# Performance work log

Hardware: AMD Instinct MI355X
Metric: run time of the kernel (lower is better)

Reference implementation:

```python
import jax, jax.numpy as jnp
import numpy as np

N_EMBED = 2048
N_HEAD = 16
N_KV_HEAD = 4
HEAD_DIM = N_EMBED // N_HEAD
REPEAT = N_HEAD // N_KV_HEAD
THETA = 10000.0


def setup_inputs() -> dict:
    key = jax.random.key(0)
    ks = jax.random.split(key, 9)
    B, T = 2, 2048
    s = 0.02
    return {
        'x': jax.random.normal(ks[0], (B, T, N_EMBED), jnp.float32),
        'Wq': jax.random.normal(ks[1], (N_EMBED, N_EMBED), jnp.float32) * s,
        'bq': jax.random.normal(ks[2], (N_EMBED,), jnp.float32) * s,
        'Wk': jax.random.normal(ks[3], (N_EMBED, N_KV_HEAD * HEAD_DIM), jnp.float32) * s,
        'bk': jax.random.normal(ks[4], (N_KV_HEAD * HEAD_DIM,), jnp.float32) * s,
        'Wv': jax.random.normal(ks[5], (N_EMBED, N_KV_HEAD * HEAD_DIM), jnp.float32) * s,
        'bv': jax.random.normal(ks[6], (N_KV_HEAD * HEAD_DIM,), jnp.float32) * s,
        'Wo': jax.random.normal(ks[7], (N_EMBED, N_EMBED), jnp.float32) * s,
        'bo': jax.random.normal(ks[8], (N_EMBED,), jnp.float32) * s,
    }


def _rope_angles(T):
    # Quirk of original: freqs exponent uses full n_embed, then sliced to head_dim//2
    freqs = THETA ** (-(jnp.arange(0, N_EMBED, 2, dtype=jnp.float32) / N_EMBED))
    freqs = freqs[: HEAD_DIM // 2]
    t = jnp.arange(T, dtype=jnp.float32)
    return jnp.outer(t, freqs)  # [T, HEAD_DIM//2]


def _apply_rope(x, cos, sin):
    # x: [B, T, H, D]; pairs are adjacent elements along D
    xr = x[..., 0::2]
    xi = x[..., 1::2]
    # cos/sin: [1, T, 1, D//2]
    or_ = xr * cos - xi * sin
    oi_ = xr * sin + xi * cos
    out = jnp.stack([or_, oi_], axis=-1).reshape(x.shape)
    # original casts rope output to bfloat16
    return out.astype(jnp.bfloat16).astype(jnp.float32)


def reference(x, Wq, bq, Wk, bk, Wv, bv, Wo, bo):
    B, T, _ = x.shape
    q = (x @ Wq + bq).reshape(B, T, N_HEAD, HEAD_DIM)
    k = (x @ Wk + bk).reshape(B, T, N_KV_HEAD, HEAD_DIM)
    v = (x @ Wv + bv).reshape(B, T, N_KV_HEAD, HEAD_DIM)

    ang = _rope_angles(T)
    cos = jnp.cos(ang)[None, :, None, :]
    sin = jnp.sin(ang)[None, :, None, :]
    xq = _apply_rope(q, cos, sin)
    xk = _apply_rope(k, cos, sin)

    xq = xq.transpose(0, 2, 1, 3)                 # [B, H, T, D]
    xk = xk.transpose(0, 2, 1, 3)                 # [B, Hkv, T, D]
    xv = v.transpose(0, 2, 1, 3)                  # [B, Hkv, T, D]
    xk = jnp.repeat(xk, REPEAT, axis=1)           # [B, H, T, D]
    xv = jnp.repeat(xv, REPEAT, axis=1)

    qk = jnp.einsum('bhtd,bhsd->bhts', xq, xk)    # [B, H, T, T]
    causal = jnp.tril(jnp.ones((T, T), dtype=bool))
    qk = jnp.where(causal[None, None], qk, -jnp.inf)
    # Quirk: scale applied AFTER softmax, using n_embed**-0.5
    attn = jax.nn.softmax(qk, axis=-1) * (N_EMBED ** -0.5)
    o = jnp.einsum('bhts,bhsd->bhtd', attn, xv)
    o = o.transpose(0, 2, 1, 3).reshape(B, T, N_EMBED)
    return o @ Wo + bo
```

## Files before the change

kernel.cpp:

```cpp
#include <hip/hip_runtime.h>
#include <stdint.h>
#include <math.h>

typedef unsigned short u16;
typedef __attribute__((ext_vector_type(8))) short short8;
typedef __attribute__((ext_vector_type(8))) _Float16 half8;
typedef __attribute__((ext_vector_type(4))) float float4v;
typedef __attribute__((ext_vector_type(16))) float float16v;
typedef __attribute__((ext_vector_type(4))) u16 ushort4v;

#define T_SEQ 2048
#define NB 2
#define NE 2048
#define NH 16
#define NKV 4
#define HD 128
#define KDIM 2048

union Frag { short8 s; half8 h; };

__device__ inline u16 f32_bf16(float f) {
    union { float f; uint32_t u; } v; v.f = f;
    uint32_t u = v.u;
    return (u16)((u + 0x7fffu + ((u >> 16) & 1u)) >> 16);
}
__device__ inline u16 f32_f16(float f) {
    union { _Float16 h; u16 u; } v; v.h = (_Float16)f;
    return v.u;
}

__device__ inline uint32_t cvtpk_bf16(float lo, float hi) {
    uint32_t r;
    asm("v_cvt_pk_bf16_f32 %0, %1, %2" : "=v"(r) : "v"(lo), "v"(hi));
    return r;
}
__device__ inline void perm32swap(uint32_t& a, uint32_t& b) {
    asm("v_permlane32_swap_b32 %0, %1" : "+v"(a), "+v"(b));
}

typedef __attribute__((address_space(1))) const void g_void;
typedef __attribute__((address_space(3))) void l_void;
#define GLOAD16(g, l) __builtin_amdgcn_global_load_lds((g_void*)(g), (l_void*)(l), 16, 0, 0)

__global__ void conv_f16(const float* __restrict__ in, u16* __restrict__ out) {
    int i = blockIdx.x * blockDim.x + threadIdx.x;
    float4 v = ((const float4*)in)[i];
    ushort4v o;
    o.x = f32_f16(v.x); o.y = f32_f16(v.y); o.z = f32_f16(v.z); o.w = f32_f16(v.w);
    *(ushort4v*)(out + (size_t)i * 4) = o;
}

template<bool TO_F16>
__global__ void transpose_convert(const float* __restrict__ in, u16* __restrict__ out,
                                  int K, int N) {
    __shared__ float tile[32][33];
    int n0 = blockIdx.x * 32, k0 = blockIdx.y * 32;
    int tx = threadIdx.x, ty = threadIdx.y;
    for (int i = 0; i < 32; i += 8)
        tile[ty + i][tx] = in[(size_t)(k0 + ty + i) * N + n0 + tx];
    __syncthreads();
    for (int i = 0; i < 32; i += 8) {
        float v = tile[tx][ty + i];
        out[(size_t)(n0 + ty + i) * K + k0 + tx] = TO_F16 ? f32_f16(v) : f32_bf16(v);
    }
}

__global__ void rope_tab(float* __restrict__ ctab, float* __restrict__ stab) {
    int i = blockIdx.x * blockDim.x + threadIdx.x;
    int t = i >> 6, j = i & 63;
    float freqf = (float)pow(10000.0, -(double)j / 1024.0);
    float angf = (float)t * freqf;
    double a = (double)angf;
    ctab[i] = (float)cos(a);
    stab[i] = (float)sin(a);
}

#define GEMM_STAGE_DECL(Asrc, Bsrc) \
    int rin = lane >> 2, ksl = lane & 3; \
    int u0r = wid * 32; \
    const u16* Ag0 = (Asrc) + (size_t)(m0 + u0r + rin) * KDIM + ksl * 8; \
    const u16* Ag1 = (Asrc) + (size_t)(m0 + u0r + 16 + rin) * KDIM + ksl * 8; \
    const u16* Bg0 = (Bsrc) + (size_t)(n0 + u0r + rin) * KDIM + ksl * 8; \
    const u16* Bg1 = (Bsrc) + (size_t)(n0 + u0r + 16 + rin) * KDIM + ksl * 8; \
    u16* Al0 = &Alds[u0r * 32]; \
    u16* Al1 = &Alds[(u0r + 16) * 32]; \
    u16* Bl0 = &Blds[u0r * 32]; \
    u16* Bl1 = &Blds[(u0r + 16) * 32];

#define GEMM_MAINLOOP(F16) \
    for (int k0 = 0; k0 < KDIM; k0 += 32) { \
        __syncthreads(); \
        GLOAD16(Ag0 + k0, Al0); \
        GLOAD16(Ag1 + k0, Al1); \
        GLOAD16(Bg0 + k0, Bl0); \
        GLOAD16(Bg1 + k0, Bl1); \
        __syncthreads(); \
        Frag af[4], bf[4]; \
        for (int i = 0; i < 4; i++) \
            af[i].s = *(const short8*)&Alds[(wr * 64 + i * 16 + l16) * 32 + quad * 8]; \
        for (int j = 0; j < 4; j++) \
            bf[j].s = *(const short8*)&Blds[(wc * 64 + j * 16 + l16) * 32 + quad * 8]; \
        for (int i = 0; i < 4; i++) \
            for (int j = 0; j < 4; j++) { \
                if (F16) \
                    acc[i][j] = __builtin_amdgcn_mfma_f32_16x16x32_f16(af[i].h, bf[j].h, acc[i][j], 0, 0, 0); \
                else \
                    acc[i][j] = __builtin_amdgcn_mfma_f32_16x16x32_bf16(af[i].s, bf[j].s, acc[i][j], 0, 0, 0); \
            } \
    }

__global__ __launch_bounds__(256)
void gemm_qkv(const u16* __restrict__ xh, const u16* __restrict__ wqt,
              const u16* __restrict__ wkt, const u16* __restrict__ wvt,
              const float* __restrict__ bq, const float* __restrict__ bk,
              const float* __restrict__ bv,
              u16* __restrict__ qout, u16* __restrict__ kout, u16* __restrict__ vout,
              const float* __restrict__ ctab, const float* __restrict__ stab) {
    __shared__ u16 Alds[128 * 32];
    __shared__ u16 Blds[128 * 32];
    int tid = threadIdx.x;
    int wid = tid >> 6, lane = tid & 63;
    int quad = lane >> 4, l16 = lane & 15;
    int wr = wid >> 1, wc = wid & 1;

    int lin = blockIdx.x;
    int mode, m0, n0;
    const u16 *A, *Bt;
    if (lin < 512) {
        mode = 0; m0 = (lin >> 4) * 128; n0 = (lin & 15) * 128; A = xh; Bt = wqt;
    } else if (lin < 640) {
        int i = lin - 512;
        mode = 1; m0 = (i >> 2) * 128; n0 = (i & 3) * 128; A = xh; Bt = wkt;
    } else {
        int i = lin - 640;
        mode = 2; m0 = (i & 3) * 128; n0 = (i >> 2) * 128; A = wvt; Bt = xh;
    }

    float4v acc[4][4];
    for (int i = 0; i < 4; i++) for (int j = 0; j < 4; j++) acc[i][j] = (float4v){0,0,0,0};

    GEMM_STAGE_DECL(A, Bt)
    GEMM_MAINLOOP(true)

    if (mode == 2) {
        for (int i = 0; i < 4; i++) {
            int mbase = m0 + wr * 64 + i * 16 + quad * 4;
            float brow[4];
            for (int r = 0; r < 4; r++) brow[r] = bv[mbase + r];
            for (int j = 0; j < 4; j++) {
                int col = n0 + wc * 64 + j * 16 + l16;
                int b = col >> 11, t = col & 2047;
                for (int r = 0; r < 4; r++) {
                    int m = mbase + r;
                    float val = acc[i][j][r] + brow[r];
                    vout[(((size_t)(b * NKV + (m >> 7))) * HD + (m & 127)) * T_SEQ + t] = f32_bf16(val);
                }
            }
        }
    } else {
        const float* bias = mode ? bk : bq;
        u16* outU = mode ? kout : qout;
        int nheads = mode ? NKV : NH;
        for (int i = 0; i < 4; i++) {
            int mbase = m0 + wr * 64 + i * 16 + quad * 4;
            for (int j = 0; j < 4; j++) {
                int col = n0 + wc * 64 + j * 16 + l16;
                float bcol = bias[col];
                for (int r = 0; r < 4; r++) {
                    int m = mbase + r;
                    float val = acc[i][j][r] + bcol;
                    int b = m >> 11, t = m & 2047;
                    int h = col >> 7, d = col & 127;
                    int jj = d >> 1;
                    float c = ctab[t * 64 + jj];
                    float s = stab[t * 64 + jj];
                    float partner = __shfl_xor(val, 1, 64);
                    float o = (d & 1) ? (partner * s + val * c) : (val * c - partner * s);
                    outU[(((size_t)(b * nheads + h)) * T_SEQ + t) * HD + d] = f32_bf16(o);
                }
            }
        }
    }
}

__global__ __launch_bounds__(256)
void gemm_out(const u16* __restrict__ A, const u16* __restrict__ Bt,
              const float* __restrict__ bias, float* __restrict__ outF) {
    __shared__ u16 Alds[128 * 32];
    __shared__ u16 Blds[128 * 32];
    int tid = threadIdx.x;
    int wid = tid >> 6, lane = tid & 63;
    int quad = lane >> 4, l16 = lane & 15;
    int wr = wid >> 1, wc = wid & 1;
    int m0 = blockIdx.x * 128, n0 = blockIdx.y * 128;

    float4v acc[4][4];
    for (int i = 0; i < 4; i++) for (int j = 0; j < 4; j++) acc[i][j] = (float4v){0,0,0,0};

    GEMM_STAGE_DECL(A, Bt)
    GEMM_MAINLOOP(false)

    for (int i = 0; i < 4; i++) {
        int mbase = m0 + wr * 64 + i * 16 + quad * 4;
        for (int j = 0; j < 4; j++) {
            int col = n0 + wc * 64 + j * 16 + l16;
            float bcol = bias[col];
            for (int r = 0; r < 4; r++)
                outF[(size_t)(mbase + r) * NE + col] = acc[i][j][r] + bcol;
        }
    }
}

__global__ __launch_bounds__(256, 2)
void attn_kernel(const u16* __restrict__ Qr, const u16* __restrict__ Kr,
                 const u16* __restrict__ Vt, u16* __restrict__ Oout) {
    __shared__ u16 smem[17920];
    u16* klds = smem;
    u16* vlds = smem + 8704;
    int tid = threadIdx.x;
    int wid = tid >> 6, lane = tid & 63;
    int l32 = lane & 31, hh = lane >> 5;

    int lin = blockIdx.x + (blockIdx.y << 4);
    int g = lin >> 5, bh = lin & 31;
    int qt = (lin < 256) ? (15 - g) : (g - 8);
    int b = bh >> 4, hd = bh & 15, kvh = hd >> 2;
    int t0 = qt * 128;

    const u16* Qb = Qr + (((size_t)(b * NH + hd)) * T_SEQ + t0 + wid * 32) * HD;
    const u16* Kb = Kr + ((size_t)(b * NKV + kvh)) * T_SEQ * HD;
    const u16* Vb = Vt + ((size_t)(b * NKV + kvh)) * HD * T_SEQ;

    short8 qf[8];
#pragma unroll
    for (int ks = 0; ks < 8; ks++)
        qf[ks] = *(const short8*)(Qb + (size_t)l32 * HD + ks * 16 + hh * 8);

    float16v oacc[4];
#pragma unroll
    for (int dt = 0; dt < 4; dt++)
        oacc[dt] = (float16v){0,0,0,0,0,0,0,0,0,0,0,0,0,0,0,0};
    float m_run = -INFINITY, l_run = 0.f;

    int ksr = tid >> 2, kc = (tid & 3) * 32;
    int vdr = tid >> 1, vc = (tid & 1) * 32;

    int nst = 2 * qt + 2;

    {
        const u16* ksrc = Kb + (size_t)ksr * HD + kc;
        const u16* vsrc = Vb + (size_t)vdr * T_SEQ + vc;
        short8 kr0[4], vr0[4];
#pragma unroll
        for (int i = 0; i < 4; i++) kr0[i] = *(const short8*)(ksrc + i * 8);
#pragma unroll
        for (int i = 0; i < 4; i++) vr0[i] = *(const short8*)(vsrc + i * 8);
#pragma unroll
        for (int i = 0; i < 4; i++) *(short8*)&klds[ksr * 136 + kc + i * 8] = kr0[i];
#pragma unroll
        for (int i = 0; i < 4; i++) *(short8*)&vlds[vdr * 72 + vc + i * 8] = vr0[i];
    }
    __syncthreads();

    for (int st = 0; st < nst; st++) {
        short8 krg[4], vrg[4];
        bool more = (st + 1 < nst);
        if (more) {
            const u16* ksrc = Kb + ((size_t)(st + 1) * 64 + ksr) * HD + kc;
            const u16* vsrc = Vb + (size_t)vdr * T_SEQ + (st + 1) * 64 + vc;
#pragma unroll
            for (int i = 0; i < 4; i++) krg[i] = *(const short8*)(ksrc + i * 8);
#pragma unroll
            for (int i = 0; i < 4; i++) vrg[i] = *(const short8*)(vsrc + i * 8);
        }

        bool active = (st * 64) <= (t0 + wid * 32 + 31);
        if (active) {
            float16v sfa[2];
            sfa[0] = (float16v){0,0,0,0,0,0,0,0,0,0,0,0,0,0,0,0};
            sfa[1] = (float16v){0,0,0,0,0,0,0,0,0,0,0,0,0,0,0,0};
            __builtin_amdgcn_s_setprio(1);
#pragma unroll
            for (int ks = 0; ks < 8; ks++) {
                short8 kf0 = *(const short8*)&klds[l32 * 136 + ks * 16 + hh * 8];
                short8 kf1 = *(const short8*)&klds[(32 + l32) * 136 + ks * 16 + hh * 8];
                sfa[0] = __builtin_amdgcn_mfma_f32_32x32x16_bf16(kf0, qf[ks], sfa[0], 0, 0, 0);
                sfa[1] = __builtin_amdgcn_mfma_f32_32x32x16_bf16(kf1, qf[ks], sfa[1], 0, 0, 0);
            }
            __builtin_amdgcn_s_setprio(0);

            int tg = t0 + wid * 32 + l32;
            if (st >= 2 * qt) {
#pragma unroll
                for (int stile = 0; stile < 2; stile++)
#pragma unroll
                    for (int r = 0; r < 16; r++) {
                        int s = st * 64 + stile * 32 + (r & 3) + 8 * (r >> 2) + 4 * hh;
                        if (s > tg) sfa[stile][r] = -INFINITY;
                    }
            }

            float mx = -INFINITY;
#pragma unroll
            for (int stile = 0; stile < 2; stile++)
#pragma unroll
                for (int r = 0; r < 16; r++) mx = fmaxf(mx, sfa[stile][r]);
            mx = fmaxf(mx, __shfl_xor(mx, 32, 64));
            bool nos = __all(mx - m_run <= 8.f);
            float mnew = nos ? m_run : fmaxf(m_run, mx);
            float alpha = nos ? 1.f : __expf(m_run - mnew);
            float psum = 0.f;
#pragma unroll
            for (int stile = 0; stile < 2; stile++)
#pragma unroll
                for (int r = 0; r < 16; r++) {
                    float p = __expf(sfa[stile][r] - mnew);
                    sfa[stile][r] = p;
                    psum += p;
                }
            psum += __shfl_xor(psum, 32, 64);
            l_run = l_run * alpha + psum;
            m_run = mnew;

            if (!nos) {
#pragma unroll
                for (int dt = 0; dt < 4; dt++)
#pragma unroll
                    for (int r = 0; r < 16; r++) oacc[dt][r] *= alpha;
            }

            __builtin_amdgcn_s_setprio(1);
#pragma unroll
            for (int g2 = 0; g2 < 4; g2++) {
                int stile = g2 >> 1, gg = g2 & 1;
                uint32_t P0 = cvtpk_bf16(sfa[stile][8 * gg + 0], sfa[stile][8 * gg + 1]);
                uint32_t P1 = cvtpk_bf16(sfa[stile][8 * gg + 2], sfa[stile][8 * gg + 3]);
                uint32_t P2 = cvtpk_bf16(sfa[stile][8 * gg + 4], sfa[stile][8 * gg + 5]);
                uint32_t P3 = cvtpk_bf16(sfa[stile][8 * gg + 6], sfa[stile][8 * gg + 7]);
                perm32swap(P0, P2);
                perm32swap(P1, P3);
                union { uint32_t w[4]; short8 s; } pf;
                pf.w[0] = P0; pf.w[1] = P1; pf.w[2] = P2; pf.w[3] = P3;
#pragma unroll
                for (int dt = 0; dt < 4; dt++) {
                    short8 vf = *(const short8*)&vlds[(dt * 32 + l32) * 72 + g2 * 16 + hh * 8];
                    oacc[dt] = __builtin_amdgcn_mfma_f32_32x32x16_bf16(vf, pf.s, oacc[dt], 0, 0, 0);
                }
            }
            __builtin_amdgcn_s_setprio(0);
        }

        __syncthreads();
        if (more) {
#pragma unroll
            for (int i = 0; i < 4; i++) *(short8*)&klds[ksr * 136 + kc + i * 8] = krg[i];
#pragma unroll
            for (int i = 0; i < 4; i++) *(short8*)&vlds[vdr * 72 + vc + i * 8] = vrg[i];
        }
        __syncthreads();
    }

    const float scale = 0.022097086912079608f;
    float sc = scale / l_run;
    u16* ow = smem + wid * 4352;
#pragma unroll
    for (int dt = 0; dt < 4; dt++)
#pragma unroll
        for (int gq = 0; gq < 4; gq++) {
            ushort4v pk;
            pk.x = f32_bf16(oacc[dt][gq * 4 + 0] * sc);
            pk.y = f32_bf16(oacc[dt][gq * 4 + 1] * sc);
            pk.z = f32_bf16(oacc[dt][gq * 4 + 2] * sc);
            pk.w = f32_bf16(oacc[dt][gq * 4 + 3] * sc);
            *(ushort4v*)&ow[l32 * 136 + dt * 32 + gq * 8 + hh * 4] = pk;
        }
    __syncthreads();
    int tl = lane >> 4, dcol = (lane & 15) * 8;
#pragma unroll
    for (int ch = 0; ch < 8; ch++) {
        int t_local = tl + ch * 4;
        short8 ov = *(const short8*)&ow[t_local * 136 + dcol];
        *(short8*)&Oout[((size_t)(b * T_SEQ) + t0 + wid * 32 + t_local) * NE + hd * HD + dcol] = ov;
    }
}

extern "C" void kernel_launch(void* const* d_in, const int* in_sizes, int n_in,
                              void* d_out, int out_size, void* d_ws, size_t ws_size,
                              hipStream_t stream) {
    const float* x  = (const float*)d_in[0];
    const float* Wq = (const float*)d_in[1];
    const float* bq = (const float*)d_in[2];
    const float* Wk = (const float*)d_in[3];
    const float* bk = (const float*)d_in[4];
    const float* Wv = (const float*)d_in[5];
    const float* bv = (const float*)d_in[6];
    const float* Wo = (const float*)d_in[7];
    const float* bo = (const float*)d_in[8];
    float* out = (float*)d_out;
    char* ws = (char*)d_ws;

    u16* xh   = (u16*)(ws);
    u16* wqt  = (u16*)(ws + 16777216);
    u16* wkt  = (u16*)(ws + 25165824);
    u16* wvt  = (u16*)(ws + 27262976);
    u16* qr   = (u16*)(ws + 29360128);
    u16* kr   = (u16*)(ws + 46137344);
    u16* vt   = (u16*)(ws + 50331648);
    float* ctab = (float*)(ws + 54525952);
    float* stab = (float*)(ws + 55050240);
    u16* ao  = xh;
    u16* wot = wqt;

    conv_f16<<<8192, 256, 0, stream>>>(x, xh);
    transpose_convert<true><<<dim3(64, 64), dim3(32, 8), 0, stream>>>(Wq, wqt, 2048, 2048);
    transpose_convert<true><<<dim3(16, 64), dim3(32, 8), 0, stream>>>(Wk, wkt, 2048, 512);
    transpose_convert<true><<<dim3(16, 64), dim3(32, 8), 0, stream>>>(Wv, wvt, 2048, 512);
    rope_tab<<<512, 256, 0, stream>>>(ctab, stab);

    gemm_qkv<<<dim3(768), 256, 0, stream>>>(xh, wqt, wkt, wvt, bq, bk, bv,
                                            qr, kr, vt, ctab, stab);

    transpose_convert<false><<<dim3(64, 64), dim3(32, 8), 0, stream>>>(Wo, wot, 2048, 2048);

    attn_kernel<<<dim3(16, 32), 256, 0, stream>>>(qr, kr, vt, ao);

    gemm_out<<<dim3(32, 16), 256, 0, stream>>>(ao, wot, bo, out);
}
```

Baseline: 337.3 us.

## Double-buffer LDS tiles in GEMM main loop to overlap loads with MFMA

```diff
diff --git a/kernel.cpp b/kernel.cpp
--- a/kernel.cpp
+++ b/kernel.cpp
@@ -81,25 +81,25 @@
     const u16* Ag0 = (Asrc) + (size_t)(m0 + u0r + rin) * KDIM + ksl * 8; \
     const u16* Ag1 = (Asrc) + (size_t)(m0 + u0r + 16 + rin) * KDIM + ksl * 8; \
     const u16* Bg0 = (Bsrc) + (size_t)(n0 + u0r + rin) * KDIM + ksl * 8; \
-    const u16* Bg1 = (Bsrc) + (size_t)(n0 + u0r + 16 + rin) * KDIM + ksl * 8; \
-    u16* Al0 = &Alds[u0r * 32]; \
-    u16* Al1 = &Alds[(u0r + 16) * 32]; \
-    u16* Bl0 = &Blds[u0r * 32]; \
-    u16* Bl1 = &Blds[(u0r + 16) * 32];
+    const u16* Bg1 = (Bsrc) + (size_t)(n0 + u0r + 16 + rin) * KDIM + ksl * 8;
+
+#define GEMM_STAGE(buf, kk) \
+    GLOAD16(Ag0 + (kk), &Alds[buf][u0r * 32]); \
+    GLOAD16(Ag1 + (kk), &Alds[buf][(u0r + 16) * 32]); \
+    GLOAD16(Bg0 + (kk), &Blds[buf][u0r * 32]); \
+    GLOAD16(Bg1 + (kk), &Blds[buf][(u0r + 16) * 32]);
 
 #define GEMM_MAINLOOP(F16) \
+    GEMM_STAGE(0, 0) \
+    __syncthreads(); \
+    { int cur = 0; \
     for (int k0 = 0; k0 < KDIM; k0 += 32) { \
-        __syncthreads(); \
-        GLOAD16(Ag0 + k0, Al0); \
-        GLOAD16(Ag1 + k0, Al1); \
-        GLOAD16(Bg0 + k0, Bl0); \
-        GLOAD16(Bg1 + k0, Bl1); \
-        __syncthreads(); \
+        if (k0 + 32 < KDIM) { GEMM_STAGE(cur ^ 1, k0 + 32) } \
         Frag af[4], bf[4]; \
         for (int i = 0; i < 4; i++) \
-            af[i].s = *(const short8*)&Alds[(wr * 64 + i * 16 + l16) * 32 + quad * 8]; \
+            af[i].s = *(const short8*)&Alds[cur][(wr * 64 + i * 16 + l16) * 32 + quad * 8]; \
         for (int j = 0; j < 4; j++) \
-            bf[j].s = *(const short8*)&Blds[(wc * 64 + j * 16 + l16) * 32 + quad * 8]; \
+            bf[j].s = *(const short8*)&Blds[cur][(wc * 64 + j * 16 + l16) * 32 + quad * 8]; \
         for (int i = 0; i < 4; i++) \
             for (int j = 0; j < 4; j++) { \
                 if (F16) \
@@ -107,7 +107,9 @@
                 else \
                     acc[i][j] = __builtin_amdgcn_mfma_f32_16x16x32_bf16(af[i].s, bf[j].s, acc[i][j], 0, 0, 0); \
             } \
-    }
+        __syncthreads(); \
+        cur ^= 1; \
+    } }
 
 __global__ __launch_bounds__(256)
 void gemm_qkv(const u16* __restrict__ xh, const u16* __restrict__ wqt,
@@ -116,8 +118,8 @@
               const float* __restrict__ bv,
               u16* __restrict__ qout, u16* __restrict__ kout, u16* __restrict__ vout,
               const float* __restrict__ ctab, const float* __restrict__ stab) {
-    __shared__ u16 Alds[128 * 32];
-    __shared__ u16 Blds[128 * 32];
+    __shared__ u16 Alds[2][128 * 32];
+    __shared__ u16 Blds[2][128 * 32];
     int tid = threadIdx.x;
     int wid = tid >> 6, lane = tid & 63;
     int quad = lane >> 4, l16 = lane & 15;
@@ -186,8 +188,8 @@
 __global__ __launch_bounds__(256)
 void gemm_out(const u16* __restrict__ A, const u16* __restrict__ Bt,
               const float* __restrict__ bias, float* __restrict__ outF) {
-    __shared__ u16 Alds[128 * 32];
-    __shared__ u16 Blds[128 * 32];
+    __shared__ u16 Alds[2][128 * 32];
+    __shared__ u16 Blds[2][128 * 32];
     int tid = threadIdx.x;
     int wid = tid >> 6, lane = tid & 63;
     int quad = lane >> 4, l16 = lane & 15;
```

Measured after the change: 350.7 us. 1.04x slower.
